# Kernel tuning notes

Measured on AMD Instinct MI355X. Metric: run time of the kernel, lower is better.

Reference implementation:

```python
import jax, jax.numpy as jnp
import numpy as np
import math

C = 256
GROUPS = 32
EPS = 1e-5

def setup_inputs() -> dict:
    key = jax.random.key(0)
    ks = jax.random.split(key, 11)
    B, H, W = 8, 64, 64
    s = 1.0 / math.sqrt(C)
    return {
        "x": jax.random.normal(ks[0], (B, C, H, W), dtype=jnp.float32),
        "gamma": jnp.ones((C,), jnp.float32),
        "beta": jnp.zeros((C,), jnp.float32),
        "wq": jax.random.normal(ks[1], (C, C), jnp.float32) * s,
        "bq": jnp.zeros((C,), jnp.float32),
        "wk": jax.random.normal(ks[2], (C, C), jnp.float32) * s,
        "bk": jnp.zeros((C,), jnp.float32),
        "wv": jax.random.normal(ks[3], (C, C), jnp.float32) * s,
        "bv": jnp.zeros((C,), jnp.float32),
        "wp": jax.random.normal(ks[4], (C, C), jnp.float32) * s,
        "bp": jnp.zeros((C,), jnp.float32),
    }

def _group_norm(x, gamma, beta):
    B, Cc, H, W = x.shape
    xg = x.reshape(B, GROUPS, Cc // GROUPS, H, W)
    mu = xg.mean(axis=(2, 3, 4), keepdims=True)
    var = xg.var(axis=(2, 3, 4), keepdims=True)
    xn = ((xg - mu) * jax.lax.rsqrt(var + EPS)).reshape(B, Cc, H, W)
    return xn * gamma[None, :, None, None] + beta[None, :, None, None]

def reference(x, gamma, beta, wq, bq, wk, bk, wv, bv, wp, bp):
    B, Cc, H, W = x.shape
    T = H * W
    h = _group_norm(x, gamma, beta)           # (B,C,H,W)
    hf = h.reshape(B, Cc, T)                  # (B,C,T)
    # 1x1 convs = per-pixel linear maps over channels
    q = jnp.einsum('oc,bct->bto', wq, hf) + bq           # (B,T,C)
    k = jnp.einsum('oc,bct->bot', wk, hf) + bk[:, None]  # (B,C,T)
    v = jnp.einsum('oc,bct->bto', wv, hf) + bv           # (B,T,C)
    scores = jnp.einsum('btc,bcs->bts', q, k) / math.sqrt(Cc)
    attn = jax.nn.softmax(scores, axis=-1)    # (B,T,T)
    z = jnp.einsum('bts,bsc->btc', attn, v)   # (B,T,C)
    zf = z.transpose(0, 2, 1)                 # (B,C,T)
    proj = jnp.einsum('oc,bct->bot', wp, zf) + bp[:, None]
    return x + proj.reshape(B, Cc, H, W)
```

## Files before the change

### kernel.cpp

```cpp
#include <hip/hip_runtime.h>


typedef unsigned short u16;
typedef __attribute__((ext_vector_type(8))) short short8;
typedef __attribute__((ext_vector_type(4))) float f32x4;

#define MFMA16(a, b, c) __builtin_amdgcn_mfma_f32_16x16x32_bf16((a), (b), (c), 0, 0, 0)

#define GLL16(g, l)                                                            \
  __builtin_amdgcn_global_load_lds(                                            \
      (const __attribute__((address_space(1))) void*)(g),                      \
      (__attribute__((address_space(3))) void*)(l), 16, 0, 0)

#define BAR_VM8()  asm volatile("s_waitcnt vmcnt(8)\n\ts_barrier" ::: "memory")
#define BAR_LGKM() asm volatile("s_waitcnt lgkmcnt(0)\n\ts_barrier" ::: "memory")

__device__ __forceinline__ u16 f2bf(float f) {
  union { float f; unsigned u; } v; v.f = f;
  unsigned u = v.u;
  return (u16)((u + 0x7FFFu + ((u >> 16) & 1u)) >> 16);
}

__global__ __launch_bounds__(256) void conv_w(const float* __restrict__ s0,
                                              const float* __restrict__ s1,
                                              const float* __restrict__ s2,
                                              const float* __restrict__ s3,
                                              u16* __restrict__ dst) {
  const int m = blockIdx.y;
  const float* s = (m == 0) ? s0 : (m == 1) ? s1 : (m == 2) ? s2 : s3;
  const int i = (blockIdx.x * 256 + threadIdx.x) * 4;
  float4 v = *(const float4*)(s + i);
  u16* d = dst + m * 65536 + i;
  d[0] = f2bf(v.x); d[1] = f2bf(v.y); d[2] = f2bf(v.z); d[3] = f2bf(v.w);
}

__global__ __launch_bounds__(256) void gn_stats(const float* __restrict__ x,
                                                float2* __restrict__ stats) {
  const int bg = blockIdx.x;
  const float* p = x + (long)bg * 32768;
  const int tid = threadIdx.x;
  float s = 0.f, ss = 0.f;
  #pragma unroll 8
  for (int i = 0; i < 32; ++i) {
    float4 v = *(const float4*)(p + tid * 4 + i * 1024);
    s  += v.x + v.y + v.z + v.w;
    ss += v.x * v.x + v.y * v.y + v.z * v.z + v.w * v.w;
  }
  for (int off = 32; off; off >>= 1) {
    s  += __shfl_down(s, off);
    ss += __shfl_down(ss, off);
  }
  __shared__ float2 red[4];
  if ((tid & 63) == 0) red[tid >> 6] = make_float2(s, ss);
  __syncthreads();
  if (tid == 0) {
    float S  = red[0].x + red[1].x + red[2].x + red[3].x;
    float SS = red[0].y + red[1].y + red[2].y + red[3].y;
    float mean = S * (1.f / 32768.f);
    float var  = SS * (1.f / 32768.f) - mean * mean;
    stats[bg] = make_float2(mean, rsqrtf(var + 1e-5f));
  }
}

__global__ __launch_bounds__(256) void gn_apply(const float* __restrict__ x,
                                                const float2* __restrict__ stats,
                                                const float* __restrict__ gamma,
                                                const float* __restrict__ beta,
                                                u16* __restrict__ h_t) {
  __shared__ float tile[64][65];
  const int tid = threadIdx.x;
  const int b = blockIdx.z, c0 = blockIdx.y * 64, t0 = blockIdx.x * 64;
  {
    const int ci = tid >> 2, tj0 = (tid & 3) * 16;
    const int c = c0 + ci;
    float2 st = stats[b * 32 + (c >> 3)];
    float gm = gamma[c] * st.y;
    float bt = beta[c] - st.x * gm;
    const float* xp = x + ((long)(b * 256 + c) * 4096 + t0 + tj0);
    #pragma unroll
    for (int i = 0; i < 4; ++i) {
      float4 v = *(const float4*)(xp + i * 4);
      tile[ci][tj0 + i * 4 + 0] = v.x * gm + bt;
      tile[ci][tj0 + i * 4 + 1] = v.y * gm + bt;
      tile[ci][tj0 + i * 4 + 2] = v.z * gm + bt;
      tile[ci][tj0 + i * 4 + 3] = v.w * gm + bt;
    }
  }
  __syncthreads();
  {
    const int tj = tid >> 2, ci0 = (tid & 3) * 16;
    u16* hp = h_t + ((long)(b * 4096 + t0 + tj) * 256 + c0 + ci0);
    short8 v0, v1;
    #pragma unroll
    for (int i = 0; i < 8; ++i) v0[i] = (short)f2bf(tile[ci0 + i][tj]);
    #pragma unroll
    for (int i = 0; i < 8; ++i) v1[i] = (short)f2bf(tile[ci0 + 8 + i][tj]);
    *(short8*)hp = v0;
    *(short8*)(hp + 8) = v1;
  }
}

template <bool ROW_BIAS, bool RESID>
__global__ __launch_bounds__(256, 2) void gemm_bt(
    const u16* __restrict__ A, long strideAz, const u16* __restrict__ B,
    long strideBz, const float* __restrict__ bias, float scale,
    u16* __restrict__ outb, float* __restrict__ outf,
    const float* __restrict__ resid, long strideOz, int N) {
  __shared__ u16 a_lds[128 * 32];
  __shared__ u16 b_lds[128 * 32];
  const int tid = threadIdx.x, w = tid >> 6, l = tid & 63;
  const int l15 = l & 15, l4 = l >> 4;
  const int bz = blockIdx.z;
  A += bz * strideAz;
  B += bz * strideBz;
  const long obase = (long)bz * strideOz;
  const int m0 = blockIdx.y * 128, n0 = blockIdx.x * 128;
  const int wm = (w >> 1) * 64, wn = (w & 1) * 64;

  f32x4 acc[4][4];
  #pragma unroll
  for (int i = 0; i < 4; ++i)
    #pragma unroll
    for (int j = 0; j < 4; ++j) acc[i][j] = (f32x4)0.f;

  for (int kt = 0; kt < 8; ++kt) {
    const int k0 = kt * 32;
    __syncthreads();
    #pragma unroll
    for (int j = 0; j < 2; ++j) {
      const int r0 = (w * 2 + j) * 16;
      const int row = r0 + (l >> 2);
      const int sg = (l & 3) ^ (row & 3);
      GLL16(A + (long)(m0 + row) * 256 + k0 + sg * 8, a_lds + r0 * 32);
      GLL16(B + (long)(n0 + row) * 256 + k0 + sg * 8, b_lds + r0 * 32);
    }
    __syncthreads();
    short8 af[4], bf[4];
    #pragma unroll
    for (int t = 0; t < 4; ++t) {
      const int ra = wm + t * 16 + l15;
      af[t] = *(const short8*)(a_lds + ra * 32 + ((l4 ^ (ra & 3)) * 8));
      const int rb = wn + t * 16 + l15;
      bf[t] = *(const short8*)(b_lds + rb * 32 + ((l4 ^ (rb & 3)) * 8));
    }
    #pragma unroll
    for (int mt = 0; mt < 4; ++mt)
      #pragma unroll
      for (int nt = 0; nt < 4; ++nt) acc[mt][nt] = MFMA16(af[mt], bf[nt], acc[mt][nt]);
  }

  if (!ROW_BIAS) {
    float bv[4];
    #pragma unroll
    for (int nt = 0; nt < 4; ++nt) bv[nt] = bias[n0 + wn + nt * 16 + l15];
    #pragma unroll
    for (int mt = 0; mt < 4; ++mt)
      #pragma unroll
      for (int nt = 0; nt < 4; ++nt)
        #pragma unroll
        for (int r = 0; r < 4; ++r) {
          const int row = m0 + wm + mt * 16 + l4 * 4 + r;
          const int col = n0 + wn + nt * 16 + l15;
          outb[obase + (long)row * N + col] = f2bf((acc[mt][nt][r] + bv[nt]) * scale);
        }
  } else {
    float bm[4][4];
    #pragma unroll
    for (int mt = 0; mt < 4; ++mt)
      #pragma unroll
      for (int r = 0; r < 4; ++r) bm[mt][r] = bias[m0 + wm + mt * 16 + l4 * 4 + r];
    #pragma unroll
    for (int mt = 0; mt < 4; ++mt)
      #pragma unroll
      for (int nt = 0; nt < 4; ++nt)
        #pragma unroll
        for (int r = 0; r < 4; ++r) {
          const int row = m0 + wm + mt * 16 + l4 * 4 + r;
          const int col = n0 + wn + nt * 16 + l15;
          const long idx = obase + (long)row * N + col;
          float v = acc[mt][nt][r] + bm[mt][r];
          if (RESID) outf[idx] = v + resid[idx];
          else       outb[idx] = f2bf(v);
        }
  }
}

__global__ __launch_bounds__(256, 2) void gemm_qk(
    const u16* __restrict__ A, const u16* __restrict__ Bw,
    const float* __restrict__ bq, const float* __restrict__ bk,
    u16* __restrict__ Qs, u16* __restrict__ Ks) {
  __shared__ u16 a_lds[128 * 32];
  __shared__ u16 b_lds[128 * 32];
  const int tid = threadIdx.x, w = tid >> 6, l = tid & 63;
  const int l15 = l & 15, l4 = l >> 4;
  const int m0 = blockIdx.y * 128, n0 = blockIdx.x * 128;
  const int wm = (w >> 1) * 64, wn = (w & 1) * 64;

  f32x4 acc[4][4];
  #pragma unroll
  for (int i = 0; i < 4; ++i)
    #pragma unroll
    for (int j = 0; j < 4; ++j) acc[i][j] = (f32x4)0.f;

  for (int kt = 0; kt < 8; ++kt) {
    const int k0 = kt * 32;
    __syncthreads();
    #pragma unroll
    for (int j = 0; j < 2; ++j) {
      const int r0 = (w * 2 + j) * 16;
      const int row = r0 + (l >> 2);
      const int sg = (l & 3) ^ (row & 3);
      GLL16(A + (long)(m0 + row) * 256 + k0 + sg * 8, a_lds + r0 * 32);
      GLL16(Bw + (long)(n0 + row) * 256 + k0 + sg * 8, b_lds + r0 * 32);
    }
    __syncthreads();
    short8 af[4], bf[4];
    #pragma unroll
    for (int t = 0; t < 4; ++t) {
      const int ra = wm + t * 16 + l15;
      af[t] = *(const short8*)(a_lds + ra * 32 + ((l4 ^ (ra & 3)) * 8));
      const int rb = wn + t * 16 + l15;
      bf[t] = *(const short8*)(b_lds + rb * 32 + ((l4 ^ (rb & 3)) * 8));
    }
    #pragma unroll
    for (int mt = 0; mt < 4; ++mt)
      #pragma unroll
      for (int nt = 0; nt < 4; ++nt) acc[mt][nt] = MFMA16(af[mt], bf[nt], acc[mt][nt]);
  }

  const bool isQ = n0 < 256;
  u16* out = isQ ? Qs : Ks;
  const float* bias = isQ ? bq : bk;
  const float scale = isQ ? 0.0625f : 1.0f;
  const int nc0 = n0 & 255;
  float bv[4];
  #pragma unroll
  for (int nt = 0; nt < 4; ++nt) bv[nt] = bias[nc0 + wn + nt * 16 + l15];
  #pragma unroll
  for (int mt = 0; mt < 4; ++mt)
    #pragma unroll
    for (int nt = 0; nt < 4; ++nt)
      #pragma unroll
      for (int r = 0; r < 4; ++r) {
        const int row = m0 + wm + mt * 16 + l4 * 4 + r;
        const int col = nc0 + wn + nt * 16 + l15;
        out[(long)row * 256 + col] = f2bf((acc[mt][nt][r] + bv[nt]) * scale);
      }
}

__global__ __launch_bounds__(256, 2) void attn_kernel(
    const u16* __restrict__ Qs, const u16* __restrict__ Ks,
    const u16* __restrict__ Vt, u16* __restrict__ Z) {
  __shared__ u16 k_lds[16384];
  __shared__ u16 v_lds[16384];
  __shared__ u16 p_lds[64 * 72];
  __shared__ float l_buf[128];

  const int tid = threadIdx.x, w = tid >> 6, l = tid & 63;
  const int l15 = l & 15, l4 = l >> 4;
  const int bid = blockIdx.x;
  const int batch = bid & 7;
  const int qt = bid >> 3;
  const int wrow0 = (w >> 1) * 32, wcolS = (w & 1) * 32, wcolO = (w & 1) * 128;
  const long qrow_base = (long)batch * 4096 + qt * 64;

  const u16* kbase = Ks + (long)batch * 4096 * 256;
  const u16* vbase = Vt + (long)batch * 256 * 4096;

  short8 qf[2][8];
  {
    const u16* qp = Qs + (qrow_base + wrow0) * 256;
    #pragma unroll
    for (int mt = 0; mt < 2; ++mt)
      #pragma unroll
      for (int ks = 0; ks < 8; ++ks)
        qf[mt][ks] = *(const short8*)(qp + (mt * 16 + l15) * 256 + ks * 32 + l4 * 8);
  }

  const int rowk = 2 * w + (l >> 5);
  const int sgk = (l & 31) ^ (rowk & 7);
  const int cvv = 8 * w + (l >> 3);
  const int sgv = (l & 7) ^ (cvv & 7);

  f32x4 o_acc[2][8];
  #pragma unroll
  for (int mt = 0; mt < 2; ++mt)
    #pragma unroll
    for (int nt = 0; nt < 8; ++nt) o_acc[mt][nt] = (f32x4)0.f;
  float rs[2][4] = {{0.f, 0.f, 0.f, 0.f}, {0.f, 0.f, 0.f, 0.f}};

  #pragma unroll
  for (int j = 0; j < 8; ++j) {
    const int r0 = (j * 4 + w) * 2;
    GLL16(kbase + (long)(r0 + (l >> 5)) * 256 + sgk * 8, k_lds + r0 * 256);
  }
  #pragma unroll
  for (int j = 0; j < 8; ++j) {
    const int c0 = (j * 4 + w) * 8;
    GLL16(vbase + (long)(c0 + (l >> 3)) * 4096 + sgv * 8, v_lds + c0 * 64);
  }

  for (int st = 0; st < 64; ++st) {
    const int snn = ((st + 1) & 63) * 64;

    BAR_VM8();

    f32x4 sacc[2][2];
    #pragma unroll
    for (int i = 0; i < 2; ++i)
      #pragma unroll
      for (int j = 0; j < 2; ++j) sacc[i][j] = (f32x4)0.f;
    #pragma unroll
    for (int ks = 0; ks < 8; ++ks) {
      short8 kf[2];
      #pragma unroll
      for (int nt = 0; nt < 2; ++nt) {
        const int row = wcolS + nt * 16 + l15;
        const int gk = (ks * 4 + l4) ^ (row & 7);
        kf[nt] = *(const short8*)(k_lds + row * 256 + gk * 8);
      }
      #pragma unroll
      for (int mt = 0; mt < 2; ++mt)
        #pragma unroll
        for (int nt = 0; nt < 2; ++nt) sacc[mt][nt] = MFMA16(qf[mt][ks], kf[nt], sacc[mt][nt]);
    }

    #pragma unroll
    for (int mt = 0; mt < 2; ++mt)
      #pragma unroll
      for (int nt = 0; nt < 2; ++nt)
        #pragma unroll
        for (int r = 0; r < 4; ++r) {
          float p = __expf(sacc[mt][nt][r]);
          rs[mt][r] += p;
          const int prow = wrow0 + mt * 16 + l4 * 4 + r;
          const int pcol = wcolS + nt * 16 + l15;
          p_lds[prow * 72 + pcol] = f2bf(p);
        }

    BAR_LGKM();

    #pragma unroll
    for (int j = 0; j < 8; ++j) {
      const int r0 = (j * 4 + w) * 2;
      GLL16(kbase + (long)(snn + r0 + (l >> 5)) * 256 + sgk * 8, k_lds + r0 * 256);
    }

    BAR_VM8();

    #pragma unroll
    for (int ks2 = 0; ks2 < 2; ++ks2) {
      short8 pa[2];
      #pragma unroll
      for (int mt = 0; mt < 2; ++mt)
        pa[mt] = *(const short8*)(p_lds + (wrow0 + mt * 16 + l15) * 72 + ks2 * 32 + l4 * 8);
      #pragma unroll
      for (int nt = 0; nt < 8; ++nt) {
        const int c = wcolO + nt * 16 + l15;
        const int gv = (ks2 * 4 + l4) ^ (c & 7);
        short8 vb = *(const short8*)(v_lds + c * 64 + gv * 8);
        #pragma unroll
        for (int mt = 0; mt < 2; ++mt) o_acc[mt][nt] = MFMA16(pa[mt], vb, o_acc[mt][nt]);
      }
    }

    BAR_LGKM();

    #pragma unroll
    for (int j = 0; j < 8; ++j) {
      const int c0 = (j * 4 + w) * 8;
      GLL16(vbase + (long)(c0 + (l >> 3)) * 4096 + snn + sgv * 8, v_lds + c0 * 64);
    }
  }

  #pragma unroll
  for (int mt = 0; mt < 2; ++mt)
    #pragma unroll
    for (int r = 0; r < 4; ++r) {
      float v = rs[mt][r];
      v += __shfl_xor(v, 1); v += __shfl_xor(v, 2);
      v += __shfl_xor(v, 4); v += __shfl_xor(v, 8);
      rs[mt][r] = v;
    }
  if (l15 == 0) {
    #pragma unroll
    for (int mt = 0; mt < 2; ++mt)
      #pragma unroll
      for (int r = 0; r < 4; ++r)
        l_buf[(w & 1) * 64 + wrow0 + mt * 16 + l4 * 4 + r] = rs[mt][r];
  }
  __syncthreads();

  #pragma unroll
  for (int mt = 0; mt < 2; ++mt) {
    float inv[4];
    #pragma unroll
    for (int r = 0; r < 4; ++r) {
      const int row = wrow0 + mt * 16 + l4 * 4 + r;
      inv[r] = 1.f / (l_buf[row] + l_buf[64 + row]);
    }
    #pragma unroll
    for (int nt = 0; nt < 8; ++nt) {
      const int col = wcolO + nt * 16 + l15;
      #pragma unroll
      for (int r = 0; r < 4; ++r) {
        const long row = qrow_base + wrow0 + mt * 16 + l4 * 4 + r;
        Z[row * 256 + col] = f2bf(o_acc[mt][nt][r] * inv[r]);
      }
    }
  }
}

extern "C" void kernel_launch(void* const* d_in, const int* in_sizes, int n_in,
                              void* d_out, int out_size, void* d_ws, size_t ws_size,
                              hipStream_t stream) {
  (void)in_sizes; (void)n_in; (void)out_size; (void)ws_size;
  const float* x     = (const float*)d_in[0];
  const float* gamma = (const float*)d_in[1];
  const float* beta  = (const float*)d_in[2];
  const float* wq    = (const float*)d_in[3];
  const float* bq    = (const float*)d_in[4];
  const float* wk    = (const float*)d_in[5];
  const float* bk    = (const float*)d_in[6];
  const float* wv    = (const float*)d_in[7];
  const float* bv    = (const float*)d_in[8];
  const float* wp    = (const float*)d_in[9];
  const float* bp    = (const float*)d_in[10];
  float* out = (float*)d_out;

  char* ws = (char*)d_ws;
  u16*    wb    = (u16*)(ws);
  float2* stats = (float2*)(ws + 524288);
  u16*    h_t   = (u16*)(ws + 526336);
  u16*    Qs    = (u16*)(ws + 17303552);
  u16*    Ks    = (u16*)(ws + 34080768);
  u16*    Vt    = (u16*)(ws + 50857984);
  u16*    Zb    = (u16*)(ws + 67635200);

  conv_w<<<dim3(64, 4), dim3(256), 0, stream>>>(wq, wk, wv, wp, wb);
  gn_stats<<<dim3(256), dim3(256), 0, stream>>>(x, stats);
  gn_apply<<<dim3(64, 4, 8), dim3(256), 0, stream>>>(x, stats, gamma, beta, h_t);

  const long sB = 4096L * 256L, sO = 256L * 4096L;
  gemm_qk<<<dim3(4, 256), dim3(256), 0, stream>>>(h_t, wb, bq, bk, Qs, Ks);
  gemm_bt<true, false><<<dim3(32, 2, 8), dim3(256), 0, stream>>>(
      wb + 2 * 65536, 0L, h_t, sB, bv, 1.0f, Vt, nullptr, nullptr, sO, 4096);

  attn_kernel<<<dim3(512), dim3(256), 0, stream>>>(Qs, Ks, Vt, Zb);

  gemm_bt<true, true><<<dim3(32, 2, 8), dim3(256), 0, stream>>>(
      wb + 3 * 65536, 0L, Zb, sB, bp, 1.0f, nullptr, out, x, sO, 4096);
}
```

Baseline: 306.5 us.

## Store Q and K in fp8 and compute attention scores with fp8 MFMA

The QK projection now writes Q and K as fp8 (each scaled by 0.25, so the product carries the 1/sqrt(C) factor) instead of bf16. The attention kernel loads K tiles into a half-size LDS buffer with a new 16-byte XOR swizzle and computes S^T with fp8 MFMAs. P is written as packed ushort4 stores, and the row-sum reduction is reorganised to match. This halves Q/K memory traffic and score-MFMA cost, at the price of fp8 precision in the attention logits, which may exceed tolerance.

```diff
diff --git a/kernel.cpp b/kernel.cpp
--- a/kernel.cpp
+++ b/kernel.cpp
@@ -2,10 +2,12 @@
 
 
 typedef unsigned short u16;
+typedef unsigned char u8;
 typedef __attribute__((ext_vector_type(8))) short short8;
 typedef __attribute__((ext_vector_type(4))) float f32x4;
 
 #define MFMA16(a, b, c) __builtin_amdgcn_mfma_f32_16x16x32_bf16((a), (b), (c), 0, 0, 0)
+#define MFMA16F8(a, b, c) __builtin_amdgcn_mfma_f32_16x16x32_fp8_fp8((a), (b), (c), 0, 0, 0)
 
 #define GLL16(g, l)                                                            \
   __builtin_amdgcn_global_load_lds(                                            \
@@ -13,12 +15,18 @@
       (__attribute__((address_space(3))) void*)(l), 16, 0, 0)
 
 #define BAR_VM8()  asm volatile("s_waitcnt vmcnt(8)\n\ts_barrier" ::: "memory")
+#define BAR_VM4()  asm volatile("s_waitcnt vmcnt(4)\n\ts_barrier" ::: "memory")
 #define BAR_LGKM() asm volatile("s_waitcnt lgkmcnt(0)\n\ts_barrier" ::: "memory")
 
 __device__ __forceinline__ u16 f2bf(float f) {
   union { float f; unsigned u; } v; v.f = f;
   unsigned u = v.u;
   return (u16)((u + 0x7FFFu + ((u >> 16) & 1u)) >> 16);
+}
+
+__device__ __forceinline__ u8 f2fp8(float f) {
+  int p = __builtin_amdgcn_cvt_pk_fp8_f32(f, f, 0, false);
+  return (u8)(p & 0xff);
 }
 
 __global__ __launch_bounds__(256) void conv_w(const float* __restrict__ s0,
@@ -188,7 +196,7 @@
 __global__ __launch_bounds__(256, 2) void gemm_qk(
     const u16* __restrict__ A, const u16* __restrict__ Bw,
     const float* __restrict__ bq, const float* __restrict__ bk,
-    u16* __restrict__ Qs, u16* __restrict__ Ks) {
+    u8* __restrict__ Qs8, u8* __restrict__ Ks8) {
   __shared__ u16 a_lds[128 * 32];
   __shared__ u16 b_lds[128 * 32];
   const int tid = threadIdx.x, w = tid >> 6, l = tid & 63;
@@ -229,9 +237,8 @@
   }
 
   const bool isQ = n0 < 256;
-  u16* out = isQ ? Qs : Ks;
+  u8* out = isQ ? Qs8 : Ks8;
   const float* bias = isQ ? bq : bk;
-  const float scale = isQ ? 0.0625f : 1.0f;
   const int nc0 = n0 & 255;
   float bv[4];
   #pragma unroll
@@ -244,41 +251,39 @@
       for (int r = 0; r < 4; ++r) {
         const int row = m0 + wm + mt * 16 + l4 * 4 + r;
         const int col = nc0 + wn + nt * 16 + l15;
-        out[(long)row * 256 + col] = f2bf((acc[mt][nt][r] + bv[nt]) * scale);
+        out[(long)row * 256 + col] = f2fp8((acc[mt][nt][r] + bv[nt]) * 0.25f);
       }
 }
 
 __global__ __launch_bounds__(256, 2) void attn_kernel(
-    const u16* __restrict__ Qs, const u16* __restrict__ Ks,
+    const u8* __restrict__ Qs8, const u8* __restrict__ Ks8,
     const u16* __restrict__ Vt, u16* __restrict__ Z) {
-  __shared__ u16 k_lds[16384];
+  __shared__ u8  k_lds8[16384];
   __shared__ u16 v_lds[16384];
   __shared__ u16 p_lds[64 * 72];
-  __shared__ float l_buf[128];
+  __shared__ float l_red[256];
 
   const int tid = threadIdx.x, w = tid >> 6, l = tid & 63;
   const int l15 = l & 15, l4 = l >> 4;
   const int bid = blockIdx.x;
   const int batch = bid & 7;
   const int qt = bid >> 3;
-  const int wrow0 = (w >> 1) * 32, wcolS = (w & 1) * 32, wcolO = (w & 1) * 128;
+  const int ws0 = (w & 1) * 32, wq0 = (w >> 1) * 32, wcolO = (w & 1) * 128;
   const long qrow_base = (long)batch * 4096 + qt * 64;
 
-  const u16* kbase = Ks + (long)batch * 4096 * 256;
+  const u8*  kbase = Ks8 + (long)batch * 4096 * 256;
   const u16* vbase = Vt + (long)batch * 256 * 4096;
 
-  short8 qf[2][8];
+  long qf[2][8];
   {
-    const u16* qp = Qs + (qrow_base + wrow0) * 256;
-    #pragma unroll
-    for (int mt = 0; mt < 2; ++mt)
+    const u8* qp = Qs8 + (qrow_base + wq0) * 256;
+    #pragma unroll
+    for (int qt2 = 0; qt2 < 2; ++qt2)
       #pragma unroll
       for (int ks = 0; ks < 8; ++ks)
-        qf[mt][ks] = *(const short8*)(qp + (mt * 16 + l15) * 256 + ks * 32 + l4 * 8);
-  }
-
-  const int rowk = 2 * w + (l >> 5);
-  const int sgk = (l & 31) ^ (rowk & 7);
+        qf[qt2][ks] = *(const long*)(qp + (qt2 * 16 + l15) * 256 + ks * 32 + l4 * 8);
+  }
+
   const int cvv = 8 * w + (l >> 3);
   const int sgv = (l & 7) ^ (cvv & 7);
 
@@ -287,12 +292,14 @@
   for (int mt = 0; mt < 2; ++mt)
     #pragma unroll
     for (int nt = 0; nt < 8; ++nt) o_acc[mt][nt] = (f32x4)0.f;
-  float rs[2][4] = {{0.f, 0.f, 0.f, 0.f}, {0.f, 0.f, 0.f, 0.f}};
-
-  #pragma unroll
-  for (int j = 0; j < 8; ++j) {
-    const int r0 = (j * 4 + w) * 2;
-    GLL16(kbase + (long)(r0 + (l >> 5)) * 256 + sgk * 8, k_lds + r0 * 256);
+  float rs2[2] = {0.f, 0.f};
+
+  #pragma unroll
+  for (int j = 0; j < 4; ++j) {
+    const int r0 = (j * 4 + w) * 4;
+    const int row = r0 + (l >> 4);
+    const int g = (l & 15) ^ (row & 15);
+    GLL16(kbase + (long)row * 256 + g * 16, k_lds8 + r0 * 256);
   }
   #pragma unroll
   for (int j = 0; j < 8; ++j) {
@@ -312,48 +319,49 @@
       for (int j = 0; j < 2; ++j) sacc[i][j] = (f32x4)0.f;
     #pragma unroll
     for (int ks = 0; ks < 8; ++ks) {
-      short8 kf[2];
-      #pragma unroll
-      for (int nt = 0; nt < 2; ++nt) {
-        const int row = wcolS + nt * 16 + l15;
-        const int gk = (ks * 4 + l4) ^ (row & 7);
-        kf[nt] = *(const short8*)(k_lds + row * 256 + gk * 8);
+      long kf[2];
+      #pragma unroll
+      for (int st2 = 0; st2 < 2; ++st2) {
+        const int row = ws0 + st2 * 16 + l15;
+        const int g = (ks * 2 + (l4 >> 1)) ^ l15;
+        kf[st2] = *(const long*)(k_lds8 + row * 256 + g * 16 + (l4 & 1) * 8);
       }
       #pragma unroll
-      for (int mt = 0; mt < 2; ++mt)
+      for (int st2 = 0; st2 < 2; ++st2)
         #pragma unroll
-        for (int nt = 0; nt < 2; ++nt) sacc[mt][nt] = MFMA16(qf[mt][ks], kf[nt], sacc[mt][nt]);
-    }
-
-    #pragma unroll
-    for (int mt = 0; mt < 2; ++mt)
-      #pragma unroll
-      for (int nt = 0; nt < 2; ++nt)
-        #pragma unroll
-        for (int r = 0; r < 4; ++r) {
-          float p = __expf(sacc[mt][nt][r]);
-          rs[mt][r] += p;
-          const int prow = wrow0 + mt * 16 + l4 * 4 + r;
-          const int pcol = wcolS + nt * 16 + l15;
-          p_lds[prow * 72 + pcol] = f2bf(p);
-        }
+        for (int qt2 = 0; qt2 < 2; ++qt2)
+          sacc[st2][qt2] = MFMA16F8(kf[st2], qf[qt2][ks], sacc[st2][qt2]);
+    }
+
+    #pragma unroll
+    for (int st2 = 0; st2 < 2; ++st2)
+      #pragma unroll
+      for (int qt2 = 0; qt2 < 2; ++qt2) {
+        float e0 = __expf(sacc[st2][qt2][0]), e1 = __expf(sacc[st2][qt2][1]);
+        float e2 = __expf(sacc[st2][qt2][2]), e3 = __expf(sacc[st2][qt2][3]);
+        rs2[qt2] += (e0 + e1) + (e2 + e3);
+        ushort4 pk = {f2bf(e0), f2bf(e1), f2bf(e2), f2bf(e3)};
+        *(ushort4*)(p_lds + (wq0 + qt2 * 16 + l15) * 72 + ws0 + st2 * 16 + l4 * 4) = pk;
+      }
 
     BAR_LGKM();
 
     #pragma unroll
-    for (int j = 0; j < 8; ++j) {
-      const int r0 = (j * 4 + w) * 2;
-      GLL16(kbase + (long)(snn + r0 + (l >> 5)) * 256 + sgk * 8, k_lds + r0 * 256);
-    }
-
-    BAR_VM8();
+    for (int j = 0; j < 4; ++j) {
+      const int r0 = (j * 4 + w) * 4;
+      const int row = r0 + (l >> 4);
+      const int g = (l & 15) ^ (row & 15);
+      GLL16(kbase + (long)(snn + row) * 256 + g * 16, k_lds8 + r0 * 256);
+    }
+
+    BAR_VM4();
 
     #pragma unroll
     for (int ks2 = 0; ks2 < 2; ++ks2) {
       short8 pa[2];
       #pragma unroll
       for (int mt = 0; mt < 2; ++mt)
-        pa[mt] = *(const short8*)(p_lds + (wrow0 + mt * 16 + l15) * 72 + ks2 * 32 + l4 * 8);
+        pa[mt] = *(const short8*)(p_lds + (wq0 + mt * 16 + l15) * 72 + ks2 * 32 + l4 * 8);
       #pragma unroll
       for (int nt = 0; nt < 8; ++nt) {
         const int c = wcolO + nt * 16 + l15;
@@ -374,20 +382,17 @@
   }
 
   #pragma unroll
-  for (int mt = 0; mt < 2; ++mt)
-    #pragma unroll
-    for (int r = 0; r < 4; ++r) {
-      float v = rs[mt][r];
-      v += __shfl_xor(v, 1); v += __shfl_xor(v, 2);
-      v += __shfl_xor(v, 4); v += __shfl_xor(v, 8);
-      rs[mt][r] = v;
-    }
-  if (l15 == 0) {
-    #pragma unroll
-    for (int mt = 0; mt < 2; ++mt)
-      #pragma unroll
-      for (int r = 0; r < 4; ++r)
-        l_buf[(w & 1) * 64 + wrow0 + mt * 16 + l4 * 4 + r] = rs[mt][r];
+  for (int qt2 = 0; qt2 < 2; ++qt2) {
+    float v = rs2[qt2];
+    v += __shfl_xor(v, 16);
+    v += __shfl_xor(v, 32);
+    if (l4 == 0) l_red[w * 64 + wq0 + qt2 * 16 + l15] = v;
+  }
+  __syncthreads();
+  if (tid < 64) {
+    const int w0 = (tid >> 5) * 2;
+    float t = l_red[w0 * 64 + tid] + l_red[(w0 + 1) * 64 + tid];
+    l_red[tid] = 1.f / t;
   }
   __syncthreads();
 
@@ -395,16 +400,13 @@
   for (int mt = 0; mt < 2; ++mt) {
     float inv[4];
     #pragma unroll
-    for (int r = 0; r < 4; ++r) {
-      const int row = wrow0 + mt * 16 + l4 * 4 + r;
-      inv[r] = 1.f / (l_buf[row] + l_buf[64 + row]);
-    }
+    for (int r = 0; r < 4; ++r) inv[r] = l_red[wq0 + mt * 16 + l4 * 4 + r];
     #pragma unroll
     for (int nt = 0; nt < 8; ++nt) {
       const int col = wcolO + nt * 16 + l15;
       #pragma unroll
       for (int r = 0; r < 4; ++r) {
-        const long row = qrow_base + wrow0 + mt * 16 + l4 * 4 + r;
+        const long row = qrow_base + wq0 + mt * 16 + l4 * 4 + r;
         Z[row * 256 + col] = f2bf(o_acc[mt][nt][r] * inv[r]);
       }
     }
@@ -432,21 +434,21 @@
   u16*    wb    = (u16*)(ws);
   float2* stats = (float2*)(ws + 524288);
   u16*    h_t   = (u16*)(ws + 526336);
-  u16*    Qs    = (u16*)(ws + 17303552);
-  u16*    Ks    = (u16*)(ws + 34080768);
-  u16*    Vt    = (u16*)(ws + 50857984);
-  u16*    Zb    = (u16*)(ws + 67635200);
+  u8*     Qs8   = (u8*)(ws + 17303552);
+  u8*     Ks8   = (u8*)(ws + 25692160);
+  u16*    Vt    = (u16*)(ws + 34080768);
+  u16*    Zb    = (u16*)(ws + 50857984);
 
   conv_w<<<dim3(64, 4), dim3(256), 0, stream>>>(wq, wk, wv, wp, wb);
   gn_stats<<<dim3(256), dim3(256), 0, stream>>>(x, stats);
   gn_apply<<<dim3(64, 4, 8), dim3(256), 0, stream>>>(x, stats, gamma, beta, h_t);
 
   const long sB = 4096L * 256L, sO = 256L * 4096L;
-  gemm_qk<<<dim3(4, 256), dim3(256), 0, stream>>>(h_t, wb, bq, bk, Qs, Ks);
+  gemm_qk<<<dim3(4, 256), dim3(256), 0, stream>>>(h_t, wb, bq, bk, Qs8, Ks8);
   gemm_bt<true, false><<<dim3(32, 2, 8), dim3(256), 0, stream>>>(
       wb + 2 * 65536, 0L, h_t, sB, bv, 1.0f, Vt, nullptr, nullptr, sO, 4096);
 
-  attn_kernel<<<dim3(512), dim3(256), 0, stream>>>(Qs, Ks, Vt, Zb);
+  attn_kernel<<<dim3(512), dim3(256), 0, stream>>>(Qs8, Ks8, Vt, Zb);
 
   gemm_bt<true, true><<<dim3(32, 2, 8), dim3(256), 0, stream>>>(
       wb + 3 * 65536, 0L, Zb, sB, bp, 1.0f, nullptr, out, x, sO, 4096);
```

Measured after the change: 295.6 us. -3.5%, faster.
